# Optimization experiments

Hardware: AMD Instinct MI355X
Metric: run time of the kernel (lower is better)

Reference implementation:

```python
import jax, jax.numpy as jnp
import numpy as np

BS, SEQ, DIM = 4, 2048, 1024
N_EXPERTS = 8


def setup_inputs() -> dict:
    key = jax.random.key(0)
    k_x, k_w, k_i = jax.random.split(key, 3)
    X = jax.random.normal(k_x, (BS, SEQ, DIM), dtype=jnp.float32)
    # trunc_normal init with std = in_features ** -0.5 (plain normal is fine for a reference)
    W = jax.random.normal(k_w, (N_EXPERTS, DIM, DIM), dtype=jnp.float32) * (DIM ** -0.5)
    indices = jax.random.randint(k_i, (BS, SEQ), 0, N_EXPERTS, dtype=jnp.int32)
    return {"X": X, "W": W, "indices": indices}


def reference(X, W, indices):
    # Y[b, s, :] = X[b, s, :] @ W[indices[b, s]].T   (F.linear semantics)
    # Dense per-expert matmuls + masked accumulate: avoids gathering a
    # [bs, seq, out, in] weight tensor; loop is over the small fixed expert count.
    n = W.shape[0]
    Y = jnp.zeros(X.shape[:2] + (W.shape[1],), dtype=X.dtype)
    for e in range(n):
        mask = (indices == e)[..., None]                      # [bs, seq, 1]
        Ye = jnp.einsum('bsd,od->bso', X, W[e])               # [bs, seq, out]
        Y = jnp.where(mask, Ye, Y)
    return Y
```

## Files before the change

kernel.cpp:

```cpp
#include <hip/hip_runtime.h>
#include <stdint.h>

#define T_TOK 8192
#define DIMK 1024
#define NEXP 8
#define BM 128
#define BN 64
#define BK 64
#define NTK (DIMK / BK)
#define MAXROWS (T_TOK + NEXP * BM)
#define MAXTILES (T_TOK / BM + NEXP)
#define NT (DIMK / BN)
#define NWG (MAXTILES * NT)

typedef __attribute__((ext_vector_type(4))) float f32x4;
typedef __attribute__((ext_vector_type(8))) short short8;
typedef __attribute__((ext_vector_type(8))) unsigned short us8;

__device__ __forceinline__ unsigned short f2bf(float f) {
  uint32_t u = __builtin_bit_cast(uint32_t, f);
  u += 0x7FFFu + ((u >> 16) & 1u);
  return (unsigned short)(u >> 16);
}

__device__ __forceinline__ void gload_lds16(const void* g, void* l) {
  __builtin_amdgcn_global_load_lds(
      (const __attribute__((address_space(1))) void*)g,
      (__attribute__((address_space(3))) void*)l, 16, 0, 0);
}

__global__ void k_prep_conv(const int* __restrict__ idx, const float* __restrict__ W,
                            const float* __restrict__ X, int* __restrict__ hdr,
                            int* __restrict__ row2tok, unsigned short* __restrict__ Wb,
                            unsigned short* __restrict__ Xb) {
  const int tid = threadIdx.x;
  const int b = blockIdx.x;
  if (b == 0) {
    __shared__ int h[NEXP];
    __shared__ int cur[NEXP];
    __shared__ int segs[NEXP + 1];
    if (tid < NEXP) h[tid] = 0;
    __syncthreads();
    for (int i = tid; i < T_TOK; i += 256) atomicAdd(&h[idx[i]], 1);
    __syncthreads();
    if (tid == 0) {
      int off = 0;
      for (int e = 0; e < NEXP; e++) {
        segs[e] = off; cur[e] = off;
        hdr[e] = h[e]; hdr[8 + e] = off;
        off += ((h[e] + BM - 1) >> 7) << 7;
      }
      segs[NEXP] = off;
    }
    __syncthreads();
    for (int e = 0; e < NEXP; e++)
      for (int p = segs[e] + h[e] + tid; p < segs[e + 1]; p += 256) row2tok[p] = -1;
    for (int p = segs[NEXP] + tid; p < MAXROWS; p += 256) row2tok[p] = -1;
    for (int i = tid; i < T_TOK; i += 256) {
      int e = idx[i];
      int pos = atomicAdd(&cur[e], 1);
      row2tok[pos] = i;
    }
    return;
  }
  const float* src;
  unsigned short* dst;
  if (b <= 4096) {
    size_t base = (size_t)(b - 1) * 2048 + tid * 8;
    src = W + base; dst = Wb + base;
  } else {
    size_t base = (size_t)(b - 4097) * 2048 + tid * 8;
    src = X + base; dst = Xb + base;
  }
  f32x4 v0 = *(const f32x4*)src;
  f32x4 v1 = *(const f32x4*)(src + 4);
  us8 o;
  o[0] = f2bf(v0[0]); o[1] = f2bf(v0[1]); o[2] = f2bf(v0[2]); o[3] = f2bf(v0[3]);
  o[4] = f2bf(v1[0]); o[5] = f2bf(v1[1]); o[6] = f2bf(v1[2]); o[7] = f2bf(v1[3]);
  *(us8*)dst = o;
}

__global__ __launch_bounds__(256, 4) void k_gemm(
    const unsigned short* __restrict__ Xb, const unsigned short* __restrict__ Wb,
    const int* __restrict__ hdr, const int* __restrict__ row2tok,
    float* __restrict__ out) {
  __shared__ unsigned short A_lds[BM * BK];
  __shared__ unsigned short B_lds[BN * BK];

  const int orig = blockIdx.x;
  const int wgid = (orig & 7) * (NWG / 8) + (orig >> 3);
  int tile = wgid >> 4;
  const int n0 = (wgid & 15) * BN;

  int e = -1, row0 = 0;
  for (int i = 0; i < NEXP; i++) {
    int te = (hdr[i] + BM - 1) >> 7;
    if (e < 0) {
      if (tile < te) { e = i; row0 = hdr[8 + i] + tile * BM; }
      else tile -= te;
    }
  }
  if (e < 0) return;

  const int tid = threadIdx.x;
  const int lane = tid & 63;
  const int wid = tid >> 6;
  const int wr = wid >> 1, wc = wid & 1;

  const int st_r = lane >> 3;
  const int st_cb = ((lane & 7) ^ st_r) << 4;

  const char* a_lane_base[4];
#pragma unroll
  for (int j = 0; j < 4; j++) {
    int r = (wid * 4 + j) * 8 + st_r;
    int tok = row2tok[row0 + r];
    if (tok < 0) tok = 0;
    a_lane_base[j] = (const char*)Xb + (size_t)tok * (DIMK * 2) + st_cb;
  }
  const char* b_base = (const char*)Wb + ((size_t)e * DIMK * DIMK + (size_t)n0 * DIMK) * 2;

  f32x4 acc[4][2];
  const f32x4 fzero = {0.f, 0.f, 0.f, 0.f};
#pragma unroll
  for (int m = 0; m < 4; m++)
#pragma unroll
    for (int n = 0; n < 2; n++) acc[m][n] = fzero;

  const int rsel = lane & 15;
  const int swz_r = (lane & 7) << 4;
  const int kgrp = (lane >> 4) << 4;

  int a_row_b[4], b_row_b[2];
#pragma unroll
  for (int m = 0; m < 4; m++) a_row_b[m] = (wr * 64 + m * 16 + rsel) * (BK * 2);
#pragma unroll
  for (int n = 0; n < 2; n++) b_row_b[n] = (wc * 32 + n * 16 + rsel) * (BK * 2);

  for (int kt = 0; kt < NTK; kt++) {
    const int k0b = kt * (BK * 2);
#pragma unroll
    for (int j = 0; j < 4; j++) {
      int c = wid * 4 + j;
      gload_lds16(a_lane_base[j] + k0b, (char*)A_lds + c * 1024);
    }
#pragma unroll
    for (int j = 0; j < 2; j++) {
      int c = wid * 2 + j;
      int r = c * 8 + st_r;
      gload_lds16(b_base + (size_t)r * (DIMK * 2) + k0b + st_cb, (char*)B_lds + c * 1024);
    }
    __syncthreads();
#pragma unroll
    for (int ks = 0; ks < 2; ks++) {
      const int kb = ks * 64 + kgrp;
      short8 av[4], bv[2];
#pragma unroll
      for (int m = 0; m < 4; m++)
        av[m] = *(const short8*)((const char*)A_lds + a_row_b[m] + (kb ^ swz_r));
#pragma unroll
      for (int n = 0; n < 2; n++)
        bv[n] = *(const short8*)((const char*)B_lds + b_row_b[n] + (kb ^ swz_r));
#pragma unroll
      for (int m = 0; m < 4; m++)
#pragma unroll
        for (int n = 0; n < 2; n++)
          acc[m][n] = __builtin_amdgcn_mfma_f32_16x16x32_bf16(av[m], bv[n], acc[m][n], 0, 0, 0);
    }
    __syncthreads();
  }

  const int rg4 = (lane >> 4) * 4;
#pragma unroll
  for (int m = 0; m < 4; m++) {
#pragma unroll
    for (int i = 0; i < 4; i++) {
      int rg = row0 + wr * 64 + m * 16 + rg4 + i;
      int tok = row2tok[rg];
      if (tok >= 0) {
        float* po = out + (size_t)tok * DIMK + n0 + wc * 32 + rsel;
#pragma unroll
        for (int n = 0; n < 2; n++) po[n * 16] = acc[m][n][i];
      }
    }
  }
}

extern "C" void kernel_launch(void* const* d_in, const int* in_sizes, int n_in,
                              void* d_out, int out_size, void* d_ws, size_t ws_size,
                              hipStream_t stream) {
  const float* X = (const float*)d_in[0];
  const float* W = (const float*)d_in[1];
  const int* idx = (const int*)d_in[2];
  float* out = (float*)d_out;
  char* ws = (char*)d_ws;

  int* hdr = (int*)ws;
  int* row2tok = (int*)(ws + 256);
  unsigned short* Wb = (unsigned short*)(ws + 65536);
  unsigned short* Xb = (unsigned short*)(ws + 65536 + 16777216);

  k_prep_conv<<<8193, 256, 0, stream>>>(idx, W, X, hdr, row2tok, Wb, Xb);
  k_gemm<<<NWG, 256, 0, stream>>>(Xb, Wb, hdr, row2tok, out);
}
```

Before: 62.04 us.

## Fuse X fp32-to-bf16 conversion into the GEMM A-tile load

The prep kernel no longer converts X to bf16 in a workspace buffer. Instead each GEMM workgroup reads fp32 X rows directly, converts them to bf16 in registers and writes them into the swizzled A LDS tile. This removes a full pass that reads 32MB and writes 16MB. In exchange, each A tile is re-read and re-converted by all 16 N-tile workgroups, doubling A load bytes per K-step (fp32 instead of bf16) and replacing async global_load_lds with register loads plus LDS stores.

```diff
diff --git a/kernel.cpp b/kernel.cpp
--- a/kernel.cpp
+++ b/kernel.cpp
@@ -30,9 +30,8 @@
 }
 
 __global__ void k_prep_conv(const int* __restrict__ idx, const float* __restrict__ W,
-                            const float* __restrict__ X, int* __restrict__ hdr,
-                            int* __restrict__ row2tok, unsigned short* __restrict__ Wb,
-                            unsigned short* __restrict__ Xb) {
+                            int* __restrict__ hdr, int* __restrict__ row2tok,
+                            unsigned short* __restrict__ Wb) {
   const int tid = threadIdx.x;
   const int b = blockIdx.x;
   if (b == 0) {
@@ -63,15 +62,9 @@
     }
     return;
   }
-  const float* src;
-  unsigned short* dst;
-  if (b <= 4096) {
-    size_t base = (size_t)(b - 1) * 2048 + tid * 8;
-    src = W + base; dst = Wb + base;
-  } else {
-    size_t base = (size_t)(b - 4097) * 2048 + tid * 8;
-    src = X + base; dst = Xb + base;
-  }
+  size_t base = (size_t)(b - 1) * 2048 + tid * 8;
+  const float* src = W + base;
+  unsigned short* dst = Wb + base;
   f32x4 v0 = *(const f32x4*)src;
   f32x4 v1 = *(const f32x4*)(src + 4);
   us8 o;
@@ -81,7 +74,7 @@
 }
 
 __global__ __launch_bounds__(256, 4) void k_gemm(
-    const unsigned short* __restrict__ Xb, const unsigned short* __restrict__ Wb,
+    const float* __restrict__ X, const unsigned short* __restrict__ Wb,
     const int* __restrict__ hdr, const int* __restrict__ row2tok,
     float* __restrict__ out) {
   __shared__ unsigned short A_lds[BM * BK];
@@ -108,15 +101,16 @@
   const int wr = wid >> 1, wc = wid & 1;
 
   const int st_r = lane >> 3;
-  const int st_cb = ((lane & 7) ^ st_r) << 4;
-
-  const char* a_lane_base[4];
+  const int swz_col8 = ((lane & 7) ^ st_r) * 8;
+  const int st_cb = swz_col8 * 2;
+
+  const float* a_src[4];
 #pragma unroll
   for (int j = 0; j < 4; j++) {
     int r = (wid * 4 + j) * 8 + st_r;
     int tok = row2tok[row0 + r];
     if (tok < 0) tok = 0;
-    a_lane_base[j] = (const char*)Xb + (size_t)tok * (DIMK * 2) + st_cb;
+    a_src[j] = X + (size_t)tok * DIMK + swz_col8;
   }
   const char* b_base = (const char*)Wb + ((size_t)e * DIMK * DIMK + (size_t)n0 * DIMK) * 2;
 
@@ -139,17 +133,27 @@
 
   for (int kt = 0; kt < NTK; kt++) {
     const int k0b = kt * (BK * 2);
-#pragma unroll
-    for (int j = 0; j < 4; j++) {
-      int c = wid * 4 + j;
-      gload_lds16(a_lane_base[j] + k0b, (char*)A_lds + c * 1024);
-    }
+    const int k0f = kt * BK;
 #pragma unroll
     for (int j = 0; j < 2; j++) {
       int c = wid * 2 + j;
       int r = c * 8 + st_r;
       gload_lds16(b_base + (size_t)r * (DIMK * 2) + k0b + st_cb, (char*)B_lds + c * 1024);
     }
+    us8 aw[4];
+#pragma unroll
+    for (int j = 0; j < 4; j++) {
+      const float* p = a_src[j] + k0f;
+      f32x4 v0 = *(const f32x4*)p;
+      f32x4 v1 = *(const f32x4*)(p + 4);
+      aw[j][0] = f2bf(v0[0]); aw[j][1] = f2bf(v0[1]);
+      aw[j][2] = f2bf(v0[2]); aw[j][3] = f2bf(v0[3]);
+      aw[j][4] = f2bf(v1[0]); aw[j][5] = f2bf(v1[1]);
+      aw[j][6] = f2bf(v1[2]); aw[j][7] = f2bf(v1[3]);
+    }
+#pragma unroll
+    for (int j = 0; j < 4; j++)
+      *(us8*)((char*)A_lds + (wid * 4 + j) * 1024 + lane * 16) = aw[j];
     __syncthreads();
 #pragma unroll
     for (int ks = 0; ks < 2; ks++) {
@@ -198,8 +202,7 @@
   int* hdr = (int*)ws;
   int* row2tok = (int*)(ws + 256);
   unsigned short* Wb = (unsigned short*)(ws + 65536);
-  unsigned short* Xb = (unsigned short*)(ws + 65536 + 16777216);
-
-  k_prep_conv<<<8193, 256, 0, stream>>>(idx, W, X, hdr, row2tok, Wb, Xb);
-  k_gemm<<<NWG, 256, 0, stream>>>(Xb, Wb, hdr, row2tok, out);
-}
+
+  k_prep_conv<<<4097, 256, 0, stream>>>(idx, W, hdr, row2tok, Wb);
+  k_gemm<<<NWG, 256, 0, stream>>>(X, Wb, hdr, row2tok, out);
+}
```

Result: slower. 73.15 us (+17.9%).

## Overlap next K-tile global-to-LDS load with current tile MFMAs

Applied to the files above, without the earlier changes.

Restructures the GEMM main loop so each K tile is read from LDS into registers first. The direct global-to-LDS loads for the next tile are then issued before the MFMAs run, so memory latency can hide behind compute while keeping a single LDS buffer. A sched_barrier keeps the compiler from reordering across the issue point. The cost is more live registers (both k-substeps held at once) and a non-unrolled loop, which could hurt occupancy at the 4-waves launch bound.

```diff
diff --git a/kernel.cpp b/kernel.cpp
--- a/kernel.cpp
+++ b/kernel.cpp
@@ -137,38 +137,51 @@
 #pragma unroll
   for (int n = 0; n < 2; n++) b_row_b[n] = (wc * 32 + n * 16 + rsel) * (BK * 2);
 
+#define STAGE(kt)                                                              \
+  {                                                                            \
+    const int k0b = (kt) * (BK * 2);                                           \
+    _Pragma("unroll") for (int j = 0; j < 4; j++) {                            \
+      int c = wid * 4 + j;                                                     \
+      gload_lds16(a_lane_base[j] + k0b, (char*)A_lds + c * 1024);              \
+    }                                                                          \
+    _Pragma("unroll") for (int j = 0; j < 2; j++) {                            \
+      int c = wid * 2 + j;                                                     \
+      int r = c * 8 + st_r;                                                    \
+      gload_lds16(b_base + (size_t)r * (DIMK * 2) + k0b + st_cb,               \
+                  (char*)B_lds + c * 1024);                                    \
+    }                                                                          \
+  }
+
+  STAGE(0);
+  __syncthreads();
+
+#pragma unroll 1
   for (int kt = 0; kt < NTK; kt++) {
-    const int k0b = kt * (BK * 2);
-#pragma unroll
-    for (int j = 0; j < 4; j++) {
-      int c = wid * 4 + j;
-      gload_lds16(a_lane_base[j] + k0b, (char*)A_lds + c * 1024);
-    }
-#pragma unroll
-    for (int j = 0; j < 2; j++) {
-      int c = wid * 2 + j;
-      int r = c * 8 + st_r;
-      gload_lds16(b_base + (size_t)r * (DIMK * 2) + k0b + st_cb, (char*)B_lds + c * 1024);
-    }
-    __syncthreads();
+    short8 av[2][4], bv[2][2];
 #pragma unroll
     for (int ks = 0; ks < 2; ks++) {
       const int kb = ks * 64 + kgrp;
-      short8 av[4], bv[2];
 #pragma unroll
       for (int m = 0; m < 4; m++)
-        av[m] = *(const short8*)((const char*)A_lds + a_row_b[m] + (kb ^ swz_r));
+        av[ks][m] = *(const short8*)((const char*)A_lds + a_row_b[m] + (kb ^ swz_r));
 #pragma unroll
       for (int n = 0; n < 2; n++)
-        bv[n] = *(const short8*)((const char*)B_lds + b_row_b[n] + (kb ^ swz_r));
+        bv[ks][n] = *(const short8*)((const char*)B_lds + b_row_b[n] + (kb ^ swz_r));
+    }
+    __syncthreads();
+    if (kt + 1 < NTK) STAGE(kt + 1);
+    __builtin_amdgcn_sched_barrier(0);
+#pragma unroll
+    for (int ks = 0; ks < 2; ks++)
 #pragma unroll
       for (int m = 0; m < 4; m++)
 #pragma unroll
         for (int n = 0; n < 2; n++)
-          acc[m][n] = __builtin_amdgcn_mfma_f32_16x16x32_bf16(av[m], bv[n], acc[m][n], 0, 0, 0);
-    }
-    __syncthreads();
-  }
+          acc[m][n] = __builtin_amdgcn_mfma_f32_16x16x32_bf16(
+              av[ks][m], bv[ks][n], acc[m][n], 0, 0, 0);
+    __syncthreads();
+  }
+#undef STAGE
 
   const int rg4 = (lane >> 4) * 4;
 #pragma unroll
```

New measurement: 68.14 us. 9.8% more time.
